# Kernel tuning notes

Measured on AMD Instinct MI355X. Metric: run time of the kernel, lower is better.

The kernel has to match this reference:

```python
import jax, jax.numpy as jnp
import numpy as np

EMBED = 3072
HEADS = 24
HEAD_DIM = EMBED // HEADS
FFN = 4 * EMBED
SEGS = (1024, 2048, 4096)
DILS = (1, 2, 4)
SEQ = 8192
BATCH = 1


def setup_inputs() -> dict:
    key = jax.random.key(0)
    ks = jax.random.split(key, 8)
    E, F = EMBED, FFN
    s = lambda k, shape, sc: (jax.random.normal(k, shape, jnp.float32) * sc)
    return {
        "x": s(ks[0], (BATCH, SEQ, E), 1.0),
        "expert_embed": s(ks[1], (1, 1, E), 0.02),
        "w_qkv": s(ks[2], (3 * E, E), E ** -0.5),
        "b_qkv": jnp.zeros((3 * E,), jnp.float32),
        "w_out": s(ks[3], (E, E), E ** -0.5),
        "b_out": jnp.zeros((E,), jnp.float32),
        "ln1_g": jnp.ones((E,), jnp.float32),
        "ln1_b": jnp.zeros((E,), jnp.float32),
        "w1": s(ks[4], (F, E), E ** -0.5),
        "b1": jnp.zeros((F,), jnp.float32),
        "w2": s(ks[5], (E, F), F ** -0.5),
        "b2": jnp.zeros((E,), jnp.float32),
        "ln2_g": jnp.ones((E,), jnp.float32),
        "ln2_b": jnp.zeros((E,), jnp.float32),
    }


def _layernorm(x, g, b):
    m = jnp.mean(x, axis=-1, keepdims=True)
    v = jnp.mean(jnp.square(x - m), axis=-1, keepdims=True)
    return (x - m) * jax.lax.rsqrt(v + 1e-5) * g + b


def _dilated_attn(q, k, v):
    # q,k,v: [b, n, h, d]; heads are partitioned across dilation groups
    b, n, h, d = q.shape
    G = len(SEGS)
    hg = h // G
    scale = 1.0 / np.sqrt(d)
    outs = []
    for i, (g, r) in enumerate(zip(SEGS, DILS)):
        off = i % r
        hs = slice(i * hg, (i + 1) * hg)

        def sel(t):
            # [b, n, h, d] -> [b, n//g, g//r, hg, d] (dilated segment view)
            return t.reshape(b, n // g, g, h, d)[:, :, off::r, hs, :]

        qi, ki, vi = sel(q), sel(k), sel(v)
        att = jnp.einsum("bsqhd,bskhd->bshqk", qi, ki) * scale
        att = jax.nn.softmax(att, axis=-1)
        oi = jnp.einsum("bshqk,bskhd->bsqhd", att, vi)
        # scatter dilated positions back; unselected positions stay zero
        buf = jnp.zeros((b, n // g, g, hg, d), q.dtype).at[:, :, off::r].set(oi)
        outs.append(buf.reshape(b, n, hg, d))
    return jnp.concatenate(outs, axis=2)  # head groups are contiguous slices


def reference(x, expert_embed, w_qkv, b_qkv, w_out, b_out,
              ln1_g, ln1_b, w1, b1, w2, b2, ln2_g, ln2_b):
    b, n, E = x.shape
    x = x + expert_embed
    qkv = x @ w_qkv.T + b_qkv
    q, k, v = [t.reshape(b, n, HEADS, HEAD_DIM) for t in jnp.split(qkv, 3, axis=-1)]
    a = _dilated_attn(q, k, v).reshape(b, n, E) @ w_out.T + b_out
    x = _layernorm(x + a, ln1_g, ln1_b)
    f = jax.nn.gelu(x @ w1.T + b1, approximate=False) @ w2.T + b2
    return _layernorm(x + f, ln2_g, ln2_b)
```

## Files before the change

kernel.cpp:

```cpp
#include <hip/hip_runtime.h>

typedef unsigned short u16;
typedef __bf16 bf16x8 __attribute__((ext_vector_type(8)));
typedef float f32x4 __attribute__((ext_vector_type(4)));
typedef u16 u16x4 __attribute__((ext_vector_type(4)));
typedef u16 u16x8 __attribute__((ext_vector_type(8)));

__device__ __forceinline__ u16 f2bf(float f) {
  union { float f; unsigned u; } v; v.f = f;
  return (u16)((v.u + 0x7fffu + ((v.u >> 16) & 1u)) >> 16);
}
__device__ __forceinline__ float b2f(u16 h) {
  union { unsigned u; float f; } v; v.u = ((unsigned)h) << 16; return v.f;
}

__device__ __forceinline__ void gld16(const void* g, void* l) {
  __builtin_amdgcn_global_load_lds(
      (const __attribute__((address_space(1))) unsigned int*)g,
      (__attribute__((address_space(3))) unsigned int*)l, 16, 0, 0);
}

#define BAR() asm volatile("s_barrier" ::: "memory")
#define VMC8() asm volatile("s_waitcnt vmcnt(8)" ::: "memory")
#define VMC6() asm volatile("s_waitcnt vmcnt(6)" ::: "memory")
#define VMC2() asm volatile("s_waitcnt vmcnt(2)" ::: "memory")
#define VMC0() asm volatile("s_waitcnt vmcnt(0)" ::: "memory")

__global__ __launch_bounds__(256) void prep_kernel(const float* __restrict__ x,
                                                   const float* __restrict__ ee,
                                                   u16* __restrict__ xb) {
  size_t i = ((size_t)blockIdx.x * 256 + threadIdx.x) * 4;
  int col = (int)(i % 3072);
  f32x4 v = *(const f32x4*)&x[i];
  f32x4 e = *(const f32x4*)&ee[col];
  v += e;
  u16x4 b = { f2bf(v[0]), f2bf(v[1]), f2bf(v[2]), f2bf(v[3]) };
  *(u16x4*)&xb[i] = b;
}

__global__ __launch_bounds__(256) void cvt_kernel(const float* __restrict__ in,
                                                  u16* __restrict__ out, size_t n) {
  size_t i = ((size_t)blockIdx.x * 256 + threadIdx.x) * 4;
  if (i >= n) return;
  f32x4 v = *(const f32x4*)&in[i];
  u16x4 b = { f2bf(v[0]), f2bf(v[1]), f2bf(v[2]), f2bf(v[3]) };
  *(u16x4*)&out[i] = b;
}

__global__ __launch_bounds__(256) void cvt_strided_kernel(const float* __restrict__ in,
                                                          u16* __restrict__ out, int k0) {
  size_t i = ((size_t)blockIdx.x * 256 + threadIdx.x) * 4;
  int n = (int)(i / 6144), k = (int)(i % 6144);
  f32x4 v = *(const f32x4*)&in[(size_t)n * 12288 + k0 + k];
  u16x4 b = { f2bf(v[0]), f2bf(v[1]), f2bf(v[2]), f2bf(v[3]) };
  *(u16x4*)&out[i] = b;
}

template<int EPI>
__global__ __launch_bounds__(512, 2) void gemm8_kernel(const u16* __restrict__ A,
                                                       const u16* __restrict__ B,
                                                       const float* __restrict__ bias,
                                                       void* __restrict__ C0,
                                                       void* __restrict__ C1,
                                                       int N, int K) {
  __shared__ __align__(16) u16 lds[65536];
  const int tid = threadIdx.x;
  const int lane = tid & 63;
  const int w = tid >> 6;
  const int lr = lane & 15, lc8 = (lane >> 4) * 8;
  const int wm128 = (w >> 2) * 128, wn64 = (w & 3) * 64;
  const int rsw = (lr & 7) << 3;

  const int ntile = N >> 8;
  int bid = blockIdx.x;
  int wg = (bid & 7) * (gridDim.x >> 3) + (bid >> 3);
  const int bm = wg / ntile, bn = wg % ntile;
  const size_t m0 = (size_t)bm << 8, n0 = (size_t)bn << 8;

  const int jsw = (tid & 7) ^ ((tid >> 3) & 7);
  const u16* gA = A + (m0 + (tid >> 3)) * (size_t)K + jsw * 8;
  const u16* gB = B + (n0 + ((tid >> 8) << 6) + ((tid >> 3) & 31)) * (size_t)K + jsw * 8;
  u16* lA = &lds[tid * 8];
  u16* lB = &lds[32768 + (((tid >> 8) << 12) | (((tid >> 3) & 31) << 6) | ((tid & 7) << 3))];

  f32x4 acc[8][4] = {};
  bf16x8 af[2][4], bfr[2][4];

  auto stageA = [&](int buf, int mh, int kk) {
    const int ro = mh * 64;
    gld16(gA + (size_t)ro * K + kk, lA + buf * 16384 + ro * 64);
    gld16(gA + (size_t)(ro + 128) * K + kk, lA + buf * 16384 + (ro + 128) * 64);
  };
  auto stageB = [&](int buf, int nh, int kk) {
    const int ro = nh * 32;
    gld16(gB + (size_t)ro * K + kk, lB + buf * 16384 + ro * 64);
    gld16(gB + (size_t)(ro + 128) * K + kk, lB + buf * 16384 + (ro + 128) * 64);
  };
  auto LA = [&](int buf, int mh) {
#pragma unroll
    for (int ks = 0; ks < 2; ++ks)
#pragma unroll
      for (int f = 0; f < 4; ++f) {
        int r = wm128 + mh * 64 + f * 16 + lr;
        af[ks][f] = *(const bf16x8*)&lds[buf * 16384 + r * 64 + ((ks * 32 + lc8) ^ rsw)];
      }
  };
  auto LBall = [&](int buf) {
#pragma unroll
    for (int ks = 0; ks < 2; ++ks)
#pragma unroll
      for (int f = 0; f < 4; ++f) {
        int r = wn64 + f * 16 + lr;
        bfr[ks][f] = *(const bf16x8*)&lds[32768 + buf * 16384 + r * 64 + ((ks * 32 + lc8) ^ rsw)];
      }
  };
  auto MMA = [&](int mh) {
    __builtin_amdgcn_s_setprio(1);
#pragma unroll
    for (int ks = 0; ks < 2; ++ks)
#pragma unroll
      for (int f = 0; f < 4; ++f)
#pragma unroll
        for (int f2 = 0; f2 < 4; ++f2)
          acc[mh * 4 + f][f2] = __builtin_amdgcn_mfma_f32_16x16x32_bf16(
              af[ks][f], bfr[ks][f2], acc[mh * 4 + f][f2], 0, 0, 0);
    __builtin_amdgcn_s_setprio(0);
  };

  stageB(0, 0, 0); stageB(0, 1, 0); stageA(0, 0, 0);
  stageA(0, 1, 0);
  stageB(1, 0, 64); stageB(1, 1, 64); stageA(1, 0, 64);
  VMC8();
  BAR();

  const int NIT = K >> 7;
  for (int it = 0; it < NIT; ++it) {
    const int kk = it << 7;
    const bool pred = (it + 1 < NIT);
    LBall(0); LA(0, 0);
    stageA(1, 1, kk + 64);
    BAR(); MMA(0); VMC8(); BAR();
    LA(0, 1);
    if (pred) { stageB(0, 0, kk + 128); stageB(0, 1, kk + 128); stageA(0, 0, kk + 128); }
    BAR(); MMA(1);
    if (pred) { VMC8(); } else { VMC2(); }
    BAR();
    LBall(1); LA(1, 0);
    if (pred) stageA(0, 1, kk + 128);
    BAR(); MMA(0);
    if (pred) { VMC8(); } else { VMC0(); }
    BAR();
    LA(1, 1);
    if (pred) { stageB(1, 0, kk + 192); stageB(1, 1, kk + 192); stageA(1, 0, kk + 192); }
    BAR(); MMA(1);
    if (pred) { VMC8(); }
    BAR();
  }

#pragma unroll
  for (int ni = 0; ni < 4; ++ni) {
    const int colL = wn64 + ni * 16 + lr;
    const size_t col = n0 + colL;
    const float bv = bias[col];
    const int ci = colL >> 3;
#pragma unroll
    for (int mi = 0; mi < 8; ++mi) {
#pragma unroll
      for (int rg = 0; rg < 4; ++rg) {
        const int rowL = wm128 + mi * 16 + (lc8 >> 1) + rg;
        float v = acc[mi][ni][rg] + bv;
        if constexpr (EPI == 2)
          v = 0.5f * v * (1.0f + erff(v * 0.7071067811865476f));
        const int fz = (rowL >> 2) & 7;
        lds[rowL * 256 + (((ci ^ fz) << 3) | (colL & 7))] = f2bf(v);
      }
    }
  }
  __syncthreads();
  const int row = tid >> 1, half = tid & 1;
  const int fro = (row >> 2) & 7;
  u16* dst;
  size_t cb;
  int ldc;
  if constexpr (EPI == 7) {
    const int sec = (n0 >= 3072);
    dst = sec ? (u16*)C1 : (u16*)C0;
    cb = n0 - (sec ? 3072 : 0);
    ldc = 3072;
  } else {
    dst = (u16*)C0; cb = n0; ldc = N;
  }
  u16* gout = dst + (m0 + row) * (size_t)ldc + cb + half * 128;
#pragma unroll
  for (int i = 0; i < 16; ++i) {
    const int ci = half * 16 + i;
    *(uint4*)&gout[i * 8] = *(const uint4*)&lds[row * 256 + ((ci ^ fro) << 3)];
  }
}

template<int EPI>
__global__ __launch_bounds__(512, 2) void gemm1p_kernel(const u16* __restrict__ A,
                                                        const u16* __restrict__ B,
                                                        const float* __restrict__ bias,
                                                        const float* __restrict__ residf,
                                                        const u16* __restrict__ residb,
                                                        const float* __restrict__ ee,
                                                        void* __restrict__ C0,
                                                        int N, int K) {
  __shared__ __align__(16) u16 lds[73728];
  const int tid = threadIdx.x;
  const int lane = tid & 63;
  const int w = tid >> 6;
  const int lr = lane & 15, lc8 = (lane >> 4) * 8;
  const int wm64 = (w >> 1) * 64;
  const int wn64 = (w & 1) * 64;
  const int rsw = (lr & 7) << 3;

  const int ntile = N >> 7;
  int bid = blockIdx.x;
  int wg = (bid & 7) * (gridDim.x >> 3) + (bid >> 3);
  const int bm = wg / ntile, bn = wg % ntile;
  const size_t m0 = (size_t)bm << 8, n0 = (size_t)bn << 7;

  const int jsw = (tid & 7) ^ ((tid >> 3) & 7);
  const u16* gA = A + (m0 + (tid >> 3)) * (size_t)K + jsw * 8;
  const u16* gB = B + (n0 + (tid >> 3)) * (size_t)K + jsw * 8;
  u16* lA = &lds[tid * 8];
  u16* lB = &lds[16384 + tid * 8];

  f32x4 acc[4][4] = {};
  bf16x8 af[2][4], bfr[2][4];

  const int NT = K >> 6;

  auto stageA2 = [&](int buf, int kk) {
    gld16(gA + kk, lA + buf * 24576);
    gld16(gA + (size_t)64 * K + kk, lA + buf * 24576 + 64 * 64);
    gld16(gA + (size_t)128 * K + kk, lA + buf * 24576 + 128 * 64);
    gld16(gA + (size_t)192 * K + kk, lA + buf * 24576 + 192 * 64);
  };
  auto stageB2 = [&](int buf, int kk) {
    gld16(gB + kk, lB + buf * 24576);
    gld16(gB + (size_t)64 * K + kk, lB + buf * 24576 + 64 * 64);
  };
  auto LA = [&](int buf) {
#pragma unroll
    for (int ks = 0; ks < 2; ++ks)
#pragma unroll
      for (int f = 0; f < 4; ++f) {
        int r = wm64 + f * 16 + lr;
        af[ks][f] = *(const bf16x8*)&lds[buf * 24576 + r * 64 + ((ks * 32 + lc8) ^ rsw)];
      }
  };
  auto LBall = [&](int buf) {
#pragma unroll
    for (int ks = 0; ks < 2; ++ks)
#pragma unroll
      for (int f = 0; f < 4; ++f) {
        int r = wn64 + f * 16 + lr;
        bfr[ks][f] = *(const bf16x8*)&lds[buf * 24576 + 16384 + r * 64 + ((ks * 32 + lc8) ^ rsw)];
      }
  };
  auto MMA = [&]() {
    __builtin_amdgcn_s_setprio(1);
#pragma unroll
    for (int ks = 0; ks < 2; ++ks)
#pragma unroll
      for (int f = 0; f < 4; ++f)
#pragma unroll
        for (int f2 = 0; f2 < 4; ++f2)
          acc[f][f2] = __builtin_amdgcn_mfma_f32_16x16x32_bf16(
              af[ks][f], bfr[ks][f2], acc[f][f2], 0, 0, 0);
    __builtin_amdgcn_s_setprio(0);
  };
  auto TILE = [&](int bc, int bs, int tt) {
    const int kk2 = (tt + 2) << 6;
    const bool p = (tt + 2) < NT;
    LA(bc); LBall(bc);
    if (p) { stageA2(bs, kk2); stageB2(bs, kk2); }
    BAR(); MMA();
    if (p) { VMC6(); } else { VMC0(); }
    BAR();
  };

  stageA2(0, 0); stageB2(0, 0);
  stageA2(1, 64); stageB2(1, 64);
  VMC6();
  BAR();

  for (int t = 0; t < NT; t += 3) {
    TILE(0, 2, t);
    TILE(1, 0, t + 1);
    TILE(2, 1, t + 2);
  }

#pragma unroll
  for (int nf = 0; nf < 4; ++nf) {
    const int colL = wn64 + nf * 16 + lr;
    const size_t col = n0 + colL;
    float bv = 0.f;
    if constexpr (EPI != 9) bv = bias[col];
    const int ci = colL >> 3;
#pragma unroll
    for (int f = 0; f < 4; ++f) {
#pragma unroll
      for (int rg = 0; rg < 4; ++rg) {
        const int rowL = wm64 + f * 16 + (lc8 >> 1) + rg;
        const size_t idx = (m0 + rowL) * (size_t)N + col;
        float v = acc[f][nf][rg] + bv;
        if constexpr (EPI == 3) v += residf[idx] + ee[col];
        if constexpr (EPI == 8) v += b2f(residb[idx]);
        if constexpr (EPI == 9) v += b2f(((const u16*)C0)[idx]);
        const int fz = (rowL >> 2) & 7;
        lds[rowL * 128 + (((ci ^ fz) << 3) | (colL & 7))] = f2bf(v);
      }
    }
  }
  __syncthreads();
  const int row = tid >> 1, half = tid & 1;
  const int fro = (row >> 2) & 7;
  u16* gout = (u16*)C0 + (m0 + row) * (size_t)N + n0 + half * 64;
#pragma unroll
  for (int i = 0; i < 8; ++i) {
    const int ci = half * 8 + i;
    *(uint4*)&gout[i * 8] = *(const uint4*)&lds[row * 128 + ((ci ^ fro) << 3)];
  }
}

__device__ __forceinline__ void decode_blk(int bid, int& grp, int& g, int& r, int& off,
                                           int& q16, int& hl, int& s) {
  if (bid < 1024)      { grp = 0; g = 1024; r = 1; off = 0; }
  else if (bid < 1536) { grp = 1; g = 2048; r = 2; off = 1; bid -= 1024; }
  else                 { grp = 2; g = 4096; r = 4; off = 2; bid -= 1536; }
  q16 = bid & 15; hl = (bid >> 4) & 7; s = bid >> 7;
}

__global__ __launch_bounds__(256) void vtrans_kernel(const u16* __restrict__ Vb,
                                                     u16* __restrict__ vtd) {
  int grp, g, r, off, jb, hl, s;
  decode_blk(blockIdx.x, grp, g, r, off, jb, hl, s);
  const int h = grp * 8 + hl;
  const size_t vbase = (size_t)((grp == 0) ? 0u : (grp == 1) ? 8388608u : 12582912u)
                       + (size_t)(s * 8 + hl) * 131072;
  __shared__ u16 t[64 * 128];
  const int tid = threadIdx.x;
#pragma unroll
  for (int i = 0; i < 4; ++i) {
    int c = tid + i * 256;
    int jj = c >> 4, c16 = c & 15;
    size_t pos = (size_t)s * g + off + (size_t)(jb * 64 + jj) * r;
    uint4 d = *(const uint4*)&Vb[pos * 3072 + h * 128 + c16 * 8];
    *(uint4*)((char*)t + jj * 256 + ((c16 * 16) ^ ((jj >> 3) << 4))) = d;
  }
  __syncthreads();
#pragma unroll
  for (int i = 0; i < 4; ++i) {
    int c = tid + i * 256;
    int dd = c >> 3, jc = c & 7;
    u16x8 vals;
#pragma unroll
    for (int q = 0; q < 8; ++q) {
      int row = jc * 8 + q;
      vals[q] = *(const u16*)((const char*)t + row * 256 + ((dd * 2) ^ (jc << 4)));
    }
    *(u16x8*)&vtd[vbase + (size_t)dd * 1024 + jb * 64 + jc * 8] = vals;
  }
}

__global__ __launch_bounds__(256) void attn_kernel(const u16* __restrict__ Qb,
                                                   const u16* __restrict__ Kb,
                                                   const u16* __restrict__ vtd,
                                                   u16* __restrict__ abuf) {
  int grp, g, r, off, qt, hl, s;
  decode_blk(blockIdx.x, grp, g, r, off, qt, hl, s);
  const int h = grp * 8 + hl;
  const size_t vbase = (size_t)((grp == 0) ? 0u : (grp == 1) ? 8388608u : 12582912u)
                       + (size_t)(s * 8 + hl) * 131072;
  const size_t segoff = (size_t)s * g + off;

  const int tid = threadIdx.x;
  const int lane = tid & 63, w = tid >> 6;
  const int lr = lane & 15, lc = lane >> 4;

  __shared__ u16 Kl[64 * 128];
  __shared__ u16 Vl[128 * 64];
  __shared__ u16 Pl[4][1024];

  const size_t qpos = segoff + (size_t)(qt * 64 + w * 16 + lr) * r;
  const u16* qrow = &Qb[qpos * 3072 + h * 128];
  bf16x8 qf[4];
#pragma unroll
  for (int kc = 0; kc < 4; ++kc) qf[kc] = *(const bf16x8*)&qrow[kc * 32 + lc * 8];

  float m_run[4], l_run[4];
  f32x4 ao[8] = {};
#pragma unroll
  for (int i = 0; i < 4; ++i) { m_run[i] = -1e30f; l_run[i] = 0.f; }

  const float scale = 0.08838834764831845f;

  for (int kt = 0; kt < 16; ++kt) {
    __syncthreads();
#pragma unroll
    for (int i = 0; i < 4; ++i) {
      int c = tid + i * 256;
      int jj = c >> 4, c16 = c & 15;
      size_t kpos = segoff + (size_t)(kt * 64 + jj) * r;
      uint4 kd = *(const uint4*)&Kb[kpos * 3072 + h * 128 + c16 * 8];
      *(uint4*)((char*)Kl + jj * 256 + ((c16 * 16) ^ ((jj & 7) << 4))) = kd;
      int dd = c >> 3, jc = c & 7;
      uint4 vd = *(const uint4*)&vtd[vbase + (size_t)dd * 1024 + kt * 64 + jc * 8];
      *(uint4*)((char*)Vl + dd * 128 + ((jc * 16) ^ ((dd & 7) << 4))) = vd;
    }
    __syncthreads();

    f32x4 sc4[4] = {};
#pragma unroll
    for (int kb = 0; kb < 4; ++kb) {
      const int key = kb * 16 + lr;
      const int swz = (key & 7) << 4;
#pragma unroll
      for (int kc = 0; kc < 4; ++kc) {
        bf16x8 kf = *(const bf16x8*)((const char*)Kl + key * 256 + ((kc * 64 + lc * 16) ^ swz));
        sc4[kb] = __builtin_amdgcn_mfma_f32_16x16x32_bf16(qf[kc], kf, sc4[kb], 0, 0, 0);
      }
    }

    float pv[4][4];
#pragma unroll
    for (int rg = 0; rg < 4; ++rg) {
      float t = fmaxf(fmaxf(sc4[0][rg], sc4[1][rg]), fmaxf(sc4[2][rg], sc4[3][rg]));
#pragma unroll
      for (int sh = 1; sh < 16; sh <<= 1) t = fmaxf(t, __shfl_xor(t, sh, 64));
      t *= scale;
      const float mn = fmaxf(m_run[rg], t);
      const float corr = __expf(m_run[rg] - mn);
      m_run[rg] = mn;
      float sum = 0.f;
#pragma unroll
      for (int kb = 0; kb < 4; ++kb) {
        float p = __expf(sc4[kb][rg] * scale - mn);
        pv[kb][rg] = p; sum += p;
      }
#pragma unroll
      for (int sh = 1; sh < 16; sh <<= 1) sum += __shfl_xor(sum, sh, 64);
      l_run[rg] = l_run[rg] * corr + sum;
#pragma unroll
      for (int nb = 0; nb < 8; ++nb) ao[nb][rg] *= corr;
    }

#pragma unroll
    for (int rg = 0; rg < 4; ++rg) {
      const int q = lc * 4 + rg;
      const int swq = (q & 7) << 4;
#pragma unroll
      for (int kb = 0; kb < 4; ++kb) {
        const int key = kb * 16 + lr;
        *(u16*)((char*)&Pl[w][0] + q * 128 + ((key * 2) ^ swq)) = f2bf(pv[kb][rg]);
      }
    }
    __syncthreads();

#pragma unroll
    for (int kc2 = 0; kc2 < 2; ++kc2) {
      bf16x8 pf = *(const bf16x8*)((const char*)&Pl[w][0] + lr * 128 + ((kc2 * 64 + lc * 16) ^ ((lr & 7) << 4)));
#pragma unroll
      for (int nb = 0; nb < 8; ++nb) {
        const int dd = nb * 16 + lr;
        bf16x8 vf = *(const bf16x8*)((const char*)Vl + dd * 128 + ((kc2 * 64 + lc * 16) ^ ((dd & 7) << 4)));
        ao[nb] = __builtin_amdgcn_mfma_f32_16x16x32_bf16(pf, vf, ao[nb], 0, 0, 0);
      }
    }
  }

#pragma unroll
  for (int rg = 0; rg < 4; ++rg) {
    const float inv = 1.f / l_run[rg];
    const size_t opos = segoff + (size_t)(qt * 64 + w * 16 + lc * 4 + rg) * r;
    u16* orow = &abuf[opos * 3072 + h * 128];
#pragma unroll
    for (int nb = 0; nb < 8; ++nb) orow[nb * 16 + lr] = f2bf(ao[nb][rg] * inv);
  }
}

template<int IN_BF, int OUT_BF>
__global__ __launch_bounds__(256) void ln_kernel(const void* __restrict__ yv,
                                                 const float* __restrict__ gm,
                                                 const float* __restrict__ bt,
                                                 void* __restrict__ outv) {
  const size_t row = blockIdx.x;
  const int tid = threadIdx.x;
  float v[12];
  float s = 0.f, ss = 0.f;
#pragma unroll
  for (int i = 0; i < 3; ++i) {
    if constexpr (IN_BF) {
      u16x4 raw = *(const u16x4*)((const u16*)yv + row * 3072 + tid * 4 + i * 1024);
#pragma unroll
      for (int j = 0; j < 4; ++j) { float f = b2f(raw[j]); v[i * 4 + j] = f; s += f; ss += f * f; }
    } else {
      f32x4 raw = *(const f32x4*)((const float*)yv + row * 3072 + tid * 4 + i * 1024);
#pragma unroll
      for (int j = 0; j < 4; ++j) { float f = raw[j]; v[i * 4 + j] = f; s += f; ss += f * f; }
    }
  }
#pragma unroll
  for (int sh = 1; sh < 64; sh <<= 1) { s += __shfl_xor(s, sh, 64); ss += __shfl_xor(ss, sh, 64); }
  __shared__ float red[8];
  if ((tid & 63) == 0) { red[tid >> 6] = s; red[4 + (tid >> 6)] = ss; }
  __syncthreads();
  s = red[0] + red[1] + red[2] + red[3];
  ss = red[4] + red[5] + red[6] + red[7];
  const float mean = s * (1.f / 3072.f);
  const float var = ss * (1.f / 3072.f) - mean * mean;
  const float rs = rsqrtf(var + 1e-5f);
#pragma unroll
  for (int i = 0; i < 3; ++i) {
    int c = tid * 4 + i * 1024;
    f32x4 g4 = *(const f32x4*)&gm[c];
    f32x4 b4 = *(const f32x4*)&bt[c];
    if constexpr (OUT_BF) {
      u16x4 ob;
#pragma unroll
      for (int j = 0; j < 4; ++j) ob[j] = f2bf((v[i * 4 + j] - mean) * rs * g4[j] + b4[j]);
      *(u16x4*)((u16*)outv + row * 3072 + c) = ob;
    } else {
      f32x4 o;
#pragma unroll
      for (int j = 0; j < 4; ++j) o[j] = (v[i * 4 + j] - mean) * rs * g4[j] + b4[j];
      *(f32x4*)((float*)outv + row * 3072 + c) = o;
    }
  }
}

extern "C" void kernel_launch(void* const* d_in, const int* in_sizes, int n_in,
                              void* d_out, int out_size, void* d_ws, size_t ws_size,
                              hipStream_t stream) {
  (void)in_sizes; (void)n_in; (void)out_size;
  const float* x    = (const float*)d_in[0];
  const float* ee   = (const float*)d_in[1];
  const float* wqkv = (const float*)d_in[2];
  const float* bqkv = (const float*)d_in[3];
  const float* wout = (const float*)d_in[4];
  const float* bout = (const float*)d_in[5];
  const float* ln1g = (const float*)d_in[6];
  const float* ln1b = (const float*)d_in[7];
  const float* w1   = (const float*)d_in[8];
  const float* b1   = (const float*)d_in[9];
  const float* w2   = (const float*)d_in[10];
  const float* b2   = (const float*)d_in[11];
  const float* ln2g = (const float*)d_in[12];
  const float* ln2b = (const float*)d_in[13];
  float* out = (float*)d_out;

  static const size_t OFF_B1  = 50331648;
  static const size_t OFF_B2  = 100663296;
  static const size_t WS_NEED = 150994944;
  if (ws_size < WS_NEED) return;

  char* ws = (char*)d_ws;
  u16*   xb    = (u16*)(ws);
  u16*   vtd   = (u16*)(ws);
  u16*   wbo   = (u16*)(ws);
  u16*   x1b   = (u16*)(ws);
  u16*   Qb    = (u16*)(ws + OFF_B1);
  u16*   y1b   = (u16*)(ws + OFF_B1);
  u16*   y2b   = (u16*)(ws + OFF_B1);
  u16*   wslot = (u16*)(ws + OFF_B2);
  u16*   abuf  = (u16*)(ws + OFF_B2);
  u16*   Kb    = (u16*)d_out;
  u16*   Vb    = (u16*)((char*)d_out + 50331648);
  u16*   hcd   = (u16*)d_out;

  prep_kernel<<<24576, 256, 0, stream>>>(x, ee, xb);

  cvt_kernel<<<18432, 256, 0, stream>>>(wqkv, wslot, 18874368);
  gemm8_kernel<7><<<768, 512, 0, stream>>>(xb, wslot, bqkv, Qb, Kb, 6144, 3072);
  cvt_kernel<<<9216, 256, 0, stream>>>(wqkv + 18874368, wslot, 9437184);
  gemm1p_kernel<0><<<768, 512, 0, stream>>>(xb, wslot, bqkv + 6144, nullptr, nullptr, nullptr,
                                            Vb, 3072, 3072);

  vtrans_kernel<<<1792, 256, 0, stream>>>(Vb, vtd);
  hipMemsetAsync(abuf, 0, 50331648, stream);
  attn_kernel<<<1792, 256, 0, stream>>>(Qb, Kb, vtd, abuf);

  cvt_kernel<<<9216, 256, 0, stream>>>(wout, wbo, 9437184);
  gemm1p_kernel<3><<<768, 512, 0, stream>>>(abuf, wbo, bout, x, nullptr, ee,
                                            y1b, 3072, 3072);
  ln_kernel<1, 1><<<8192, 256, 0, stream>>>(y1b, ln1g, ln1b, x1b);

  for (int c = 0; c < 2; ++c) {
    cvt_kernel<<<18432, 256, 0, stream>>>(w1 + (size_t)c * 18874368, wslot, 18874368);
    gemm8_kernel<2><<<768, 512, 0, stream>>>(x1b, wslot, b1 + c * 6144, hcd, nullptr, 6144, 3072);
    cvt_strided_kernel<<<18432, 256, 0, stream>>>(w2, wslot, c * 6144);
    if (c == 0)
      gemm1p_kernel<8><<<768, 512, 0, stream>>>(hcd, wslot, b2, nullptr, x1b, nullptr,
                                                y2b, 3072, 6144);
    else
      gemm1p_kernel<9><<<768, 512, 0, stream>>>(hcd, wslot, b2, nullptr, nullptr, nullptr,
                                                y2b, 3072, 6144);
  }

  ln_kernel<1, 0><<<8192, 256, 0, stream>>>(y2b, ln2g, ln2b, out);
}
```

Baseline: 2.318 ms.

## Unify GEMMs onto the 256x128-tile kernel and drop a pre-MMA barrier

Removes the 256x256-tile gemm8 kernel and routes the QKV and FFN1 GEMMs through the smaller-tile gemm1p-style kernel, now renamed gemmu. That kernel gains the GELU epilogue and the split Q/K output. Those launches double their grid to 1536 blocks. The change also drops the barrier before MMA in the pipelined tile loop to cut synchronisation stalls. The smaller tiles give more blocks and better load balance but less operand reuse per block, and removing the barrier risks an LDS read/write race unless the wait-count ordering still covers it.

```diff
diff --git a/kernel.cpp b/kernel.cpp
--- a/kernel.cpp
+++ b/kernel.cpp
@@ -21,9 +21,7 @@
 }
 
 #define BAR() asm volatile("s_barrier" ::: "memory")
-#define VMC8() asm volatile("s_waitcnt vmcnt(8)" ::: "memory")
 #define VMC6() asm volatile("s_waitcnt vmcnt(6)" ::: "memory")
-#define VMC2() asm volatile("s_waitcnt vmcnt(2)" ::: "memory")
 #define VMC0() asm volatile("s_waitcnt vmcnt(0)" ::: "memory")
 
 __global__ __launch_bounds__(256) void prep_kernel(const float* __restrict__ x,
@@ -57,156 +55,15 @@
 }
 
 template<int EPI>
-__global__ __launch_bounds__(512, 2) void gemm8_kernel(const u16* __restrict__ A,
+__global__ __launch_bounds__(512, 2) void gemmu_kernel(const u16* __restrict__ A,
                                                        const u16* __restrict__ B,
                                                        const float* __restrict__ bias,
+                                                       const float* __restrict__ residf,
+                                                       const u16* __restrict__ residb,
+                                                       const float* __restrict__ ee,
                                                        void* __restrict__ C0,
                                                        void* __restrict__ C1,
                                                        int N, int K) {
-  __shared__ __align__(16) u16 lds[65536];
-  const int tid = threadIdx.x;
-  const int lane = tid & 63;
-  const int w = tid >> 6;
-  const int lr = lane & 15, lc8 = (lane >> 4) * 8;
-  const int wm128 = (w >> 2) * 128, wn64 = (w & 3) * 64;
-  const int rsw = (lr & 7) << 3;
-
-  const int ntile = N >> 8;
-  int bid = blockIdx.x;
-  int wg = (bid & 7) * (gridDim.x >> 3) + (bid >> 3);
-  const int bm = wg / ntile, bn = wg % ntile;
-  const size_t m0 = (size_t)bm << 8, n0 = (size_t)bn << 8;
-
-  const int jsw = (tid & 7) ^ ((tid >> 3) & 7);
-  const u16* gA = A + (m0 + (tid >> 3)) * (size_t)K + jsw * 8;
-  const u16* gB = B + (n0 + ((tid >> 8) << 6) + ((tid >> 3) & 31)) * (size_t)K + jsw * 8;
-  u16* lA = &lds[tid * 8];
-  u16* lB = &lds[32768 + (((tid >> 8) << 12) | (((tid >> 3) & 31) << 6) | ((tid & 7) << 3))];
-
-  f32x4 acc[8][4] = {};
-  bf16x8 af[2][4], bfr[2][4];
-
-  auto stageA = [&](int buf, int mh, int kk) {
-    const int ro = mh * 64;
-    gld16(gA + (size_t)ro * K + kk, lA + buf * 16384 + ro * 64);
-    gld16(gA + (size_t)(ro + 128) * K + kk, lA + buf * 16384 + (ro + 128) * 64);
-  };
-  auto stageB = [&](int buf, int nh, int kk) {
-    const int ro = nh * 32;
-    gld16(gB + (size_t)ro * K + kk, lB + buf * 16384 + ro * 64);
-    gld16(gB + (size_t)(ro + 128) * K + kk, lB + buf * 16384 + (ro + 128) * 64);
-  };
-  auto LA = [&](int buf, int mh) {
-#pragma unroll
-    for (int ks = 0; ks < 2; ++ks)
-#pragma unroll
-      for (int f = 0; f < 4; ++f) {
-        int r = wm128 + mh * 64 + f * 16 + lr;
-        af[ks][f] = *(const bf16x8*)&lds[buf * 16384 + r * 64 + ((ks * 32 + lc8) ^ rsw)];
-      }
-  };
-  auto LBall = [&](int buf) {
-#pragma unroll
-    for (int ks = 0; ks < 2; ++ks)
-#pragma unroll
-      for (int f = 0; f < 4; ++f) {
-        int r = wn64 + f * 16 + lr;
-        bfr[ks][f] = *(const bf16x8*)&lds[32768 + buf * 16384 + r * 64 + ((ks * 32 + lc8) ^ rsw)];
-      }
-  };
-  auto MMA = [&](int mh) {
-    __builtin_amdgcn_s_setprio(1);
-#pragma unroll
-    for (int ks = 0; ks < 2; ++ks)
-#pragma unroll
-      for (int f = 0; f < 4; ++f)
-#pragma unroll
-        for (int f2 = 0; f2 < 4; ++f2)
-          acc[mh * 4 + f][f2] = __builtin_amdgcn_mfma_f32_16x16x32_bf16(
-              af[ks][f], bfr[ks][f2], acc[mh * 4 + f][f2], 0, 0, 0);
-    __builtin_amdgcn_s_setprio(0);
-  };
-
-  stageB(0, 0, 0); stageB(0, 1, 0); stageA(0, 0, 0);
-  stageA(0, 1, 0);
-  stageB(1, 0, 64); stageB(1, 1, 64); stageA(1, 0, 64);
-  VMC8();
-  BAR();
-
-  const int NIT = K >> 7;
-  for (int it = 0; it < NIT; ++it) {
-    const int kk = it << 7;
-    const bool pred = (it + 1 < NIT);
-    LBall(0); LA(0, 0);
-    stageA(1, 1, kk + 64);
-    BAR(); MMA(0); VMC8(); BAR();
-    LA(0, 1);
-    if (pred) { stageB(0, 0, kk + 128); stageB(0, 1, kk + 128); stageA(0, 0, kk + 128); }
-    BAR(); MMA(1);
-    if (pred) { VMC8(); } else { VMC2(); }
-    BAR();
-    LBall(1); LA(1, 0);
-    if (pred) stageA(0, 1, kk + 128);
-    BAR(); MMA(0);
-    if (pred) { VMC8(); } else { VMC0(); }
-    BAR();
-    LA(1, 1);
-    if (pred) { stageB(1, 0, kk + 192); stageB(1, 1, kk + 192); stageA(1, 0, kk + 192); }
-    BAR(); MMA(1);
-    if (pred) { VMC8(); }
-    BAR();
-  }
-
-#pragma unroll
-  for (int ni = 0; ni < 4; ++ni) {
-    const int colL = wn64 + ni * 16 + lr;
-    const size_t col = n0 + colL;
-    const float bv = bias[col];
-    const int ci = colL >> 3;
-#pragma unroll
-    for (int mi = 0; mi < 8; ++mi) {
-#pragma unroll
-      for (int rg = 0; rg < 4; ++rg) {
-        const int rowL = wm128 + mi * 16 + (lc8 >> 1) + rg;
-        float v = acc[mi][ni][rg] + bv;
-        if constexpr (EPI == 2)
-          v = 0.5f * v * (1.0f + erff(v * 0.7071067811865476f));
-        const int fz = (rowL >> 2) & 7;
-        lds[rowL * 256 + (((ci ^ fz) << 3) | (colL & 7))] = f2bf(v);
-      }
-    }
-  }
-  __syncthreads();
-  const int row = tid >> 1, half = tid & 1;
-  const int fro = (row >> 2) & 7;
-  u16* dst;
-  size_t cb;
-  int ldc;
-  if constexpr (EPI == 7) {
-    const int sec = (n0 >= 3072);
-    dst = sec ? (u16*)C1 : (u16*)C0;
-    cb = n0 - (sec ? 3072 : 0);
-    ldc = 3072;
-  } else {
-    dst = (u16*)C0; cb = n0; ldc = N;
-  }
-  u16* gout = dst + (m0 + row) * (size_t)ldc + cb + half * 128;
-#pragma unroll
-  for (int i = 0; i < 16; ++i) {
-    const int ci = half * 16 + i;
-    *(uint4*)&gout[i * 8] = *(const uint4*)&lds[row * 256 + ((ci ^ fro) << 3)];
-  }
-}
-
-template<int EPI>
-__global__ __launch_bounds__(512, 2) void gemm1p_kernel(const u16* __restrict__ A,
-                                                        const u16* __restrict__ B,
-                                                        const float* __restrict__ bias,
-                                                        const float* __restrict__ residf,
-                                                        const u16* __restrict__ residb,
-                                                        const float* __restrict__ ee,
-                                                        void* __restrict__ C0,
-                                                        int N, int K) {
   __shared__ __align__(16) u16 lds[73728];
   const int tid = threadIdx.x;
   const int lane = tid & 63;
@@ -278,7 +135,7 @@
     const bool p = (tt + 2) < NT;
     LA(bc); LBall(bc);
     if (p) { stageA2(bs, kk2); stageB2(bs, kk2); }
-    BAR(); MMA();
+    MMA();
     if (p) { VMC6(); } else { VMC0(); }
     BAR();
   };
@@ -294,6 +151,7 @@
     TILE(2, 1, t + 2);
   }
 
+  const int ldc = (EPI == 7) ? 3072 : N;
 #pragma unroll
   for (int nf = 0; nf < 4; ++nf) {
     const int colL = wn64 + nf * 16 + lr;
@@ -308,6 +166,8 @@
         const int rowL = wm64 + f * 16 + (lc8 >> 1) + rg;
         const size_t idx = (m0 + rowL) * (size_t)N + col;
         float v = acc[f][nf][rg] + bv;
+        if constexpr (EPI == 2)
+          v = 0.5f * v * (1.0f + erff(v * 0.7071067811865476f));
         if constexpr (EPI == 3) v += residf[idx] + ee[col];
         if constexpr (EPI == 8) v += b2f(residb[idx]);
         if constexpr (EPI == 9) v += b2f(((const u16*)C0)[idx]);
@@ -319,7 +179,16 @@
   __syncthreads();
   const int row = tid >> 1, half = tid & 1;
   const int fro = (row >> 2) & 7;
-  u16* gout = (u16*)C0 + (m0 + row) * (size_t)N + n0 + half * 64;
+  u16* dst;
+  size_t cb;
+  if constexpr (EPI == 7) {
+    const int sec = (n0 >= 3072);
+    dst = sec ? (u16*)C1 : (u16*)C0;
+    cb = n0 - (sec ? 3072 : 0);
+  } else {
+    dst = (u16*)C0; cb = n0;
+  }
+  u16* gout = dst + (m0 + row) * (size_t)ldc + cb + half * 64;
 #pragma unroll
   for (int i = 0; i < 8; ++i) {
     const int ci = half * 8 + i;
@@ -575,30 +444,32 @@
   prep_kernel<<<24576, 256, 0, stream>>>(x, ee, xb);
 
   cvt_kernel<<<18432, 256, 0, stream>>>(wqkv, wslot, 18874368);
-  gemm8_kernel<7><<<768, 512, 0, stream>>>(xb, wslot, bqkv, Qb, Kb, 6144, 3072);
+  gemmu_kernel<7><<<1536, 512, 0, stream>>>(xb, wslot, bqkv, nullptr, nullptr, nullptr,
+                                            Qb, Kb, 6144, 3072);
   cvt_kernel<<<9216, 256, 0, stream>>>(wqkv + 18874368, wslot, 9437184);
-  gemm1p_kernel<0><<<768, 512, 0, stream>>>(xb, wslot, bqkv + 6144, nullptr, nullptr, nullptr,
-                                            Vb, 3072, 3072);
+  gemmu_kernel<0><<<768, 512, 0, stream>>>(xb, wslot, bqkv + 6144, nullptr, nullptr, nullptr,
+                                           Vb, nullptr, 3072, 3072);
 
   vtrans_kernel<<<1792, 256, 0, stream>>>(Vb, vtd);
   hipMemsetAsync(abuf, 0, 50331648, stream);
   attn_kernel<<<1792, 256, 0, stream>>>(Qb, Kb, vtd, abuf);
 
   cvt_kernel<<<9216, 256, 0, stream>>>(wout, wbo, 9437184);
-  gemm1p_kernel<3><<<768, 512, 0, stream>>>(abuf, wbo, bout, x, nullptr, ee,
-                                            y1b, 3072, 3072);
+  gemmu_kernel<3><<<768, 512, 0, stream>>>(abuf, wbo, bout, x, nullptr, ee,
+                                           y1b, nullptr, 3072, 3072);
   ln_kernel<1, 1><<<8192, 256, 0, stream>>>(y1b, ln1g, ln1b, x1b);
 
   for (int c = 0; c < 2; ++c) {
     cvt_kernel<<<18432, 256, 0, stream>>>(w1 + (size_t)c * 18874368, wslot, 18874368);
-    gemm8_kernel<2><<<768, 512, 0, stream>>>(x1b, wslot, b1 + c * 6144, hcd, nullptr, 6144, 3072);
+    gemmu_kernel<2><<<1536, 512, 0, stream>>>(x1b, wslot, b1 + c * 6144, nullptr, nullptr, nullptr,
+                                              hcd, nullptr, 6144, 3072);
     cvt_strided_kernel<<<18432, 256, 0, stream>>>(w2, wslot, c * 6144);
     if (c == 0)
-      gemm1p_kernel<8><<<768, 512, 0, stream>>>(hcd, wslot, b2, nullptr, x1b, nullptr,
-                                                y2b, 3072, 6144);
+      gemmu_kernel<8><<<768, 512, 0, stream>>>(hcd, wslot, b2, nullptr, x1b, nullptr,
+                                               y2b, nullptr, 3072, 6144);
     else
-      gemm1p_kernel<9><<<768, 512, 0, stream>>>(hcd, wslot, b2, nullptr, nullptr, nullptr,
-                                                y2b, 3072, 6144);
+      gemmu_kernel<9><<<768, 512, 0, stream>>>(hcd, wslot, b2, nullptr, nullptr, nullptr,
+                                               y2b, nullptr, 3072, 6144);
   }
 
   ln_kernel<1, 0><<<8192, 256, 0, stream>>>(y2b, ln2g, ln2b, out);
```

Measured after the change: 2.276 ms. Within noise of the previous version (-1.8%).
